# Performance work log

Measured on AMD Instinct MI355X. Metric: run time of the kernel, lower is better.

## Reference

```python
import jax, jax.numpy as jnp
import numpy as np

B, NI, NO = 32, 64, 64


def setup_inputs() -> dict:
    key = jax.random.key(0)
    k1, k2, k3, k4, k5, k6 = jax.random.split(key, 6)
    return {
        "input_re": jax.random.normal(k1, (B, NI, NI), dtype=jnp.float32),
        "input_im": jax.random.normal(k2, (B, NI, NI), dtype=jnp.float32),
        "w_re": jax.random.normal(k3, (NI, NI, NO, NO), dtype=jnp.float32),
        "w_im": jax.random.normal(k4, (NI, NI, NO, NO), dtype=jnp.float32),
        "amp_weights": jax.random.normal(k5, (NI, NI), dtype=jnp.float32),
        "phase_weights": jax.random.normal(k6, (NI, NI), dtype=jnp.float32),
    }


def reference(input_re, input_im, w_re, w_im, amp_weights, phase_weights):
    # complex input field (B, NI, NI) and diffraction kernel (NI, NI, NO, NO)
    e_in = jax.lax.complex(input_re, input_im)
    w_ip = jax.lax.complex(w_re, w_im)
    # passive transmission coefficients: sigmoid(amp) * exp(i*phase)
    ts = (jax.nn.sigmoid(amp_weights)
          * jnp.exp(1j * phase_weights.astype(jnp.complex64))).astype(jnp.complex64)
    # modulated field, then sum over input pixels (i,j) -> complex GEMM
    modulated = e_in * ts[None, :, :]                    # (B, NI, NI)
    out = jnp.einsum('bij,ijkl->bkl', modulated, w_ip)   # (B, NO, NO)
    return out
```

## Files before the change

### kernel.cpp

```cpp
#include <hip/hip_runtime.h>
#include <cstdint>
#include <cstddef>

#define KC 4096
#define NN 4096
#define NB 32
#define HALF (NB * NN)

typedef __attribute__((ext_vector_type(8))) short  bf16x8;
typedef __attribute__((ext_vector_type(16))) float f32x16;

__device__ __forceinline__ unsigned short f2bf(float f) {
    union { float f; unsigned u; } v; v.f = f;
    unsigned r = v.u + 0x7fffu + ((v.u >> 16) & 1u);
    return (unsigned short)(r >> 16);
}

__global__ __launch_bounds__(256) void prep_kernel(
    const float* __restrict__ in_re, const float* __restrict__ in_im,
    const float* __restrict__ amp,   const float* __restrict__ phase,
    uint32_t* __restrict__ wsA)
{
    int tid = blockIdx.x * 256 + threadIdx.x;
    int b = tid >> 12;
    int k = tid & (KC - 1);
    float er = in_re[tid], ei = in_im[tid];
    float a = amp[k], p = phase[k];
    float s = 1.0f / (1.0f + __expf(-a));
    float sn = __sinf(p);
    float cs = __cosf(p);
    float tr = s * cs, ti = s * sn;
    float mr = er * tr - ei * ti;
    float mi = er * ti + ei * tr;
    uint32_t pk = (uint32_t)f2bf(mr) | ((uint32_t)f2bf(mi) << 16);
    wsA[((((k >> 2) << 5) + b) << 2) | (k & 3)] = pk;
}

__global__ __launch_bounds__(256, 4) void gemm_kernel(
    const float* __restrict__ w_re, const float* __restrict__ w_im,
    const uint32_t* __restrict__ wsA, float2* __restrict__ wsP, int steps)
{
    __shared__ float    ldsW[2][2][8][128];
    __shared__ uint32_t ldsA[2][256];

    const int tid  = threadIdx.x;
    const int lane = tid & 63;
    const int wave = tid >> 6;
    const int h    = lane >> 5;
    const int l32  = lane & 31;
    const int n    = blockIdx.x * 128 + wave * 32 + l32;
    const int s    = blockIdx.y;
    const int kbase = s * (steps * 8);

    const int row8 = tid >> 5;
    const int nof  = (tid & 31) << 2;
    const float* gre = w_re + (size_t)(kbase + row8) * NN + blockIdx.x * 128 + nof;
    const float* gim = w_im + (size_t)(kbase + row8) * NN + blockIdx.x * 128 + nof;
    const uint32_t* ga = wsA + (size_t)(kbase >> 2) * 128 + tid;

    f32x16 accR = {};
    f32x16 accI = {};

    auto STAGE = [&](int t, int bb) {
        __builtin_amdgcn_global_load_lds(
            (const __attribute__((address_space(1))) void*)(gre + (size_t)t * 8 * NN),
            (__attribute__((address_space(3))) void*)(&ldsW[bb][0][2 * wave][0]),
            16, 0, 0);
        __builtin_amdgcn_global_load_lds(
            (const __attribute__((address_space(1))) void*)(gim + (size_t)t * 8 * NN),
            (__attribute__((address_space(3))) void*)(&ldsW[bb][1][2 * wave][0]),
            16, 0, 0);
        __builtin_amdgcn_global_load_lds(
            (const __attribute__((address_space(1))) void*)(ga + (size_t)t * 256),
            (__attribute__((address_space(3))) void*)(&ldsA[bb][wave * 64]),
            4, 0, 0);
    };

    auto COMPUTE = [&](int bb) {
        bf16x8 afrag = *(const bf16x8*)&ldsA[bb][h * 128 + l32 * 4];
        const float* Lre = &ldsW[bb][0][h * 4][wave * 32 + l32];
        const float* Lim = &ldsW[bb][1][h * 4][wave * 32 + l32];
        float r0 = Lre[0], r1 = Lre[128], r2 = Lre[256], r3 = Lre[384];
        float i0 = Lim[0], i1 = Lim[128], i2 = Lim[256], i3 = Lim[384];

        bf16x8 bR, bI;
        bR[0] = (short)f2bf(r0);  bR[1] = (short)f2bf(-i0);
        bR[2] = (short)f2bf(r1);  bR[3] = (short)f2bf(-i1);
        bR[4] = (short)f2bf(r2);  bR[5] = (short)f2bf(-i2);
        bR[6] = (short)f2bf(r3);  bR[7] = (short)f2bf(-i3);
        bI[0] = (short)f2bf(i0);  bI[1] = (short)f2bf(r0);
        bI[2] = (short)f2bf(i1);  bI[3] = (short)f2bf(r1);
        bI[4] = (short)f2bf(i2);  bI[5] = (short)f2bf(r2);
        bI[6] = (short)f2bf(i3);  bI[7] = (short)f2bf(r3);

        accR = __builtin_amdgcn_mfma_f32_32x32x16_bf16(afrag, bR, accR, 0, 0, 0);
        accI = __builtin_amdgcn_mfma_f32_32x32x16_bf16(afrag, bI, accI, 0, 0, 0);
    };

    STAGE(0, 0);
    for (int t = 0; t < steps - 1; ++t) {
        STAGE(t + 1, (t + 1) & 1);
        asm volatile("s_waitcnt vmcnt(3)" ::: "memory");
        __builtin_amdgcn_s_barrier();
        COMPUTE(t & 1);
        __builtin_amdgcn_s_barrier();
    }
    asm volatile("s_waitcnt vmcnt(0)" ::: "memory");
    __builtin_amdgcn_s_barrier();
    COMPUTE((steps - 1) & 1);

#pragma unroll
    for (int r = 0; r < 16; ++r) {
        int brow = (r & 3) + 8 * (r >> 2) + 4 * h;
        float2 v; v.x = accR[r]; v.y = accI[r];
        wsP[((size_t)s * NB + brow) * NN + n] = v;
    }
}

__global__ __launch_bounds__(256) void reduce_kernel(
    const float4* __restrict__ wsP, float* __restrict__ out, int S)
{
    int tid = blockIdx.x * 256 + threadIdx.x;
    float re0 = 0.f, im0 = 0.f, re1 = 0.f, im1 = 0.f;
#pragma unroll 8
    for (int s = 0; s < S; ++s) {
        float4 v = wsP[(size_t)s * (NB * NN / 2) + tid];
        re0 += v.x; im0 += v.y; re1 += v.z; im1 += v.w;
    }
    float2* o_re = (float2*)out + tid;
    float2* o_im = (float2*)(out + HALF) + tid;
    *o_re = make_float2(re0, re1);
    *o_im = make_float2(im0, im1);
}

extern "C" void kernel_launch(void* const* d_in, const int* in_sizes, int n_in,
                              void* d_out, int out_size, void* d_ws, size_t ws_size,
                              hipStream_t stream)
{
    const float* in_re  = (const float*)d_in[0];
    const float* in_im  = (const float*)d_in[1];
    const float* w_re   = (const float*)d_in[2];
    const float* w_im   = (const float*)d_in[3];
    const float* amp    = (const float*)d_in[4];
    const float* phase  = (const float*)d_in[5];

    const size_t A_BYTES = (size_t)1024 * 32 * 16;
    uint32_t* wsA = (uint32_t*)d_ws;
    float2*   wsP = (float2*)((char*)d_ws + A_BYTES);

    int S = 32;
    while (S > 1 && A_BYTES + (size_t)S * NB * NN * sizeof(float2) > ws_size) S >>= 1;
    int steps = (KC / S) / 8;

    prep_kernel<<<dim3((NB * KC) / 256), dim3(256), 0, stream>>>(
        in_re, in_im, amp, phase, wsA);

    gemm_kernel<<<dim3(NN / 128, S), dim3(256), 0, stream>>>(
        w_re, w_im, wsA, wsP, steps);

    reduce_kernel<<<dim3((NB * NN / 2) / 256), dim3(256), 0, stream>>>(
        (const float4*)wsP, (float*)d_out, S);
}
```

Before: 170.8 us.

## Deepen GEMM LDS prefetch pipeline to eight buffers and halve split-K

```diff
diff --git a/kernel.cpp b/kernel.cpp
--- a/kernel.cpp
+++ b/kernel.cpp
@@ -6,6 +6,9 @@
 #define NN 4096
 #define NB 32
 #define HALF (NB * NN)
+
+#define NBUF  8
+#define DEPTH 7
 
 typedef __attribute__((ext_vector_type(8))) short  bf16x8;
 typedef __attribute__((ext_vector_type(16))) float f32x16;
@@ -36,12 +39,12 @@
     wsA[((((k >> 2) << 5) + b) << 2) | (k & 3)] = pk;
 }
 
-__global__ __launch_bounds__(256, 4) void gemm_kernel(
+__global__ __launch_bounds__(256, 2) void gemm_kernel(
     const float* __restrict__ w_re, const float* __restrict__ w_im,
     const uint32_t* __restrict__ wsA, float2* __restrict__ wsP, int steps)
 {
-    __shared__ float    ldsW[2][2][8][128];
-    __shared__ uint32_t ldsA[2][256];
+    __shared__ float    ldsW[NBUF][2][8][128];
+    __shared__ uint32_t ldsA[NBUF][256];
 
     const int tid  = threadIdx.x;
     const int lane = tid & 63;
@@ -61,22 +64,25 @@
     f32x16 accR = {};
     f32x16 accI = {};
 
-    auto STAGE = [&](int t, int bb) {
+    auto STAGE = [&](int t) {
+        int tt = t < steps ? t : steps - 1;
+        int bb = t & (NBUF - 1);
         __builtin_amdgcn_global_load_lds(
-            (const __attribute__((address_space(1))) void*)(gre + (size_t)t * 8 * NN),
+            (const __attribute__((address_space(1))) void*)(gre + (size_t)tt * 8 * NN),
             (__attribute__((address_space(3))) void*)(&ldsW[bb][0][2 * wave][0]),
             16, 0, 0);
         __builtin_amdgcn_global_load_lds(
-            (const __attribute__((address_space(1))) void*)(gim + (size_t)t * 8 * NN),
+            (const __attribute__((address_space(1))) void*)(gim + (size_t)tt * 8 * NN),
             (__attribute__((address_space(3))) void*)(&ldsW[bb][1][2 * wave][0]),
             16, 0, 0);
         __builtin_amdgcn_global_load_lds(
-            (const __attribute__((address_space(1))) void*)(ga + (size_t)t * 256),
+            (const __attribute__((address_space(1))) void*)(ga + (size_t)tt * 256),
             (__attribute__((address_space(3))) void*)(&ldsA[bb][wave * 64]),
             4, 0, 0);
     };
 
-    auto COMPUTE = [&](int bb) {
+    auto COMPUTE = [&](int t) {
+        int bb = t & (NBUF - 1);
         bf16x8 afrag = *(const bf16x8*)&ldsA[bb][h * 128 + l32 * 4];
         const float* Lre = &ldsW[bb][0][h * 4][wave * 32 + l32];
         const float* Lim = &ldsW[bb][1][h * 4][wave * 32 + l32];
@@ -97,17 +103,20 @@
         accI = __builtin_amdgcn_mfma_f32_32x32x16_bf16(afrag, bI, accI, 0, 0, 0);
     };
 
-    STAGE(0, 0);
-    for (int t = 0; t < steps - 1; ++t) {
-        STAGE(t + 1, (t + 1) & 1);
-        asm volatile("s_waitcnt vmcnt(3)" ::: "memory");
+#pragma unroll
+    for (int t = 0; t < DEPTH; ++t) STAGE(t);
+
+    for (int t = 0; t < steps - DEPTH; ++t) {
+        STAGE(t + DEPTH);
+        asm volatile("s_waitcnt vmcnt(21)" ::: "memory");
         __builtin_amdgcn_s_barrier();
-        COMPUTE(t & 1);
+        COMPUTE(t);
         __builtin_amdgcn_s_barrier();
     }
+
     asm volatile("s_waitcnt vmcnt(0)" ::: "memory");
     __builtin_amdgcn_s_barrier();
-    COMPUTE((steps - 1) & 1);
+    for (int t = steps - DEPTH; t < steps; ++t) COMPUTE(t);
 
 #pragma unroll
     for (int r = 0; r < 16; ++r) {
@@ -148,7 +157,7 @@
     uint32_t* wsA = (uint32_t*)d_ws;
     float2*   wsP = (float2*)((char*)d_ws + A_BYTES);
 
-    int S = 32;
+    int S = 16;
     while (S > 1 && A_BYTES + (size_t)S * NB * NN * sizeof(float2) > ws_size) S >>= 1;
     int steps = (KC / S) / 8;
 
```

New measurement: 166.5 us. 1.03x faster.

## Widen GEMM tiles to 256 columns and 32-deep K stages with 512 threads

Applied to the files above, without the earlier changes.

```diff
diff --git a/kernel.cpp b/kernel.cpp
--- a/kernel.cpp
+++ b/kernel.cpp
@@ -6,6 +6,7 @@
 #define NN 4096
 #define NB 32
 #define HALF (NB * NN)
+#define KB 32
 
 typedef __attribute__((ext_vector_type(8))) short  bf16x8;
 typedef __attribute__((ext_vector_type(16))) float f32x16;
@@ -36,71 +37,86 @@
     wsA[((((k >> 2) << 5) + b) << 2) | (k & 3)] = pk;
 }
 
-__global__ __launch_bounds__(256, 4) void gemm_kernel(
+__global__ __launch_bounds__(512) void gemm_kernel(
     const float* __restrict__ w_re, const float* __restrict__ w_im,
     const uint32_t* __restrict__ wsA, float2* __restrict__ wsP, int steps)
 {
-    __shared__ float    ldsW[2][2][8][128];
-    __shared__ uint32_t ldsA[2][256];
+    __shared__ float    ldsW[2][2][KB][256];
+    __shared__ uint32_t ldsA[2][KB * 32];
 
     const int tid  = threadIdx.x;
     const int lane = tid & 63;
     const int wave = tid >> 6;
     const int h    = lane >> 5;
     const int l32  = lane & 31;
-    const int n    = blockIdx.x * 128 + wave * 32 + l32;
+    const int n    = blockIdx.x * 256 + wave * 32 + l32;
     const int s    = blockIdx.y;
-    const int kbase = s * (steps * 8);
+    const int kbase = s * (steps * KB);
 
-    const int row8 = tid >> 5;
-    const int nof  = (tid & 31) << 2;
-    const float* gre = w_re + (size_t)(kbase + row8) * NN + blockIdx.x * 128 + nof;
-    const float* gim = w_im + (size_t)(kbase + row8) * NN + blockIdx.x * 128 + nof;
-    const uint32_t* ga = wsA + (size_t)(kbase >> 2) * 128 + tid;
+    const float* gW_re = w_re + (size_t)kbase * NN + blockIdx.x * 256 + (lane << 2);
+    const float* gW_im = w_im + (size_t)kbase * NN + blockIdx.x * 256 + (lane << 2);
+    const uint32_t* gA = wsA + (size_t)(kbase >> 2) * 128 + lane;
 
     f32x16 accR = {};
     f32x16 accI = {};
 
     auto STAGE = [&](int t, int bb) {
-        __builtin_amdgcn_global_load_lds(
-            (const __attribute__((address_space(1))) void*)(gre + (size_t)t * 8 * NN),
-            (__attribute__((address_space(3))) void*)(&ldsW[bb][0][2 * wave][0]),
-            16, 0, 0);
-        __builtin_amdgcn_global_load_lds(
-            (const __attribute__((address_space(1))) void*)(gim + (size_t)t * 8 * NN),
-            (__attribute__((address_space(3))) void*)(&ldsW[bb][1][2 * wave][0]),
-            16, 0, 0);
-        __builtin_amdgcn_global_load_lds(
-            (const __attribute__((address_space(1))) void*)(ga + (size_t)t * 256),
-            (__attribute__((address_space(3))) void*)(&ldsA[bb][wave * 64]),
-            4, 0, 0);
+#pragma unroll
+        for (int j = 0; j < 4; ++j) {
+            int row = j * 8 + wave;
+            __builtin_amdgcn_global_load_lds(
+                (const __attribute__((address_space(1))) void*)(gW_re + (size_t)(t * KB + row) * NN),
+                (__attribute__((address_space(3))) void*)(&ldsW[bb][0][row][0]),
+                16, 0, 0);
+        }
+#pragma unroll
+        for (int j = 0; j < 4; ++j) {
+            int row = j * 8 + wave;
+            __builtin_amdgcn_global_load_lds(
+                (const __attribute__((address_space(1))) void*)(gW_im + (size_t)(t * KB + row) * NN),
+                (__attribute__((address_space(3))) void*)(&ldsW[bb][1][row][0]),
+                16, 0, 0);
+        }
+#pragma unroll
+        for (int j = 0; j < 2; ++j) {
+            int c = wave * 2 + j;
+            __builtin_amdgcn_global_load_lds(
+                (const __attribute__((address_space(1))) void*)(gA + (size_t)t * (KB * 32) + c * 64),
+                (__attribute__((address_space(3))) void*)(&ldsA[bb][c * 64]),
+                4, 0, 0);
+        }
     };
 
     auto COMPUTE = [&](int bb) {
-        bf16x8 afrag = *(const bf16x8*)&ldsA[bb][h * 128 + l32 * 4];
-        const float* Lre = &ldsW[bb][0][h * 4][wave * 32 + l32];
-        const float* Lim = &ldsW[bb][1][h * 4][wave * 32 + l32];
-        float r0 = Lre[0], r1 = Lre[128], r2 = Lre[256], r3 = Lre[384];
-        float i0 = Lim[0], i1 = Lim[128], i2 = Lim[256], i3 = Lim[384];
+#pragma unroll
+        for (int ss = 0; ss < 4; ++ss) {
+            bf16x8 afrag = *(const bf16x8*)&ldsA[bb][ss * 256 + h * 128 + l32 * 4];
+            const float* Lre = &ldsW[bb][0][ss * 8 + h * 4][wave * 32 + l32];
+            const float* Lim = &ldsW[bb][1][ss * 8 + h * 4][wave * 32 + l32];
+            float r0 = Lre[0], r1 = Lre[256], r2 = Lre[512], r3 = Lre[768];
+            float i0 = Lim[0], i1 = Lim[256], i2 = Lim[512], i3 = Lim[768];
 
-        bf16x8 bR, bI;
-        bR[0] = (short)f2bf(r0);  bR[1] = (short)f2bf(-i0);
-        bR[2] = (short)f2bf(r1);  bR[3] = (short)f2bf(-i1);
-        bR[4] = (short)f2bf(r2);  bR[5] = (short)f2bf(-i2);
-        bR[6] = (short)f2bf(r3);  bR[7] = (short)f2bf(-i3);
-        bI[0] = (short)f2bf(i0);  bI[1] = (short)f2bf(r0);
-        bI[2] = (short)f2bf(i1);  bI[3] = (short)f2bf(r1);
-        bI[4] = (short)f2bf(i2);  bI[5] = (short)f2bf(r2);
-        bI[6] = (short)f2bf(i3);  bI[7] = (short)f2bf(r3);
+            unsigned short br0 = f2bf(r0), br1 = f2bf(r1), br2 = f2bf(r2), br3 = f2bf(r3);
+            unsigned short bi0 = f2bf(i0), bi1 = f2bf(i1), bi2 = f2bf(i2), bi3 = f2bf(i3);
+            bf16x8 bR, bI;
+            bR[0] = (short)br0;  bR[1] = (short)(bi0 ^ 0x8000);
+            bR[2] = (short)br1;  bR[3] = (short)(bi1 ^ 0x8000);
+            bR[4] = (short)br2;  bR[5] = (short)(bi2 ^ 0x8000);
+            bR[6] = (short)br3;  bR[7] = (short)(bi3 ^ 0x8000);
+            bI[0] = (short)bi0;  bI[1] = (short)br0;
+            bI[2] = (short)bi1;  bI[3] = (short)br1;
+            bI[4] = (short)bi2;  bI[5] = (short)br2;
+            bI[6] = (short)bi3;  bI[7] = (short)br3;
 
-        accR = __builtin_amdgcn_mfma_f32_32x32x16_bf16(afrag, bR, accR, 0, 0, 0);
-        accI = __builtin_amdgcn_mfma_f32_32x32x16_bf16(afrag, bI, accI, 0, 0, 0);
+            accR = __builtin_amdgcn_mfma_f32_32x32x16_bf16(afrag, bR, accR, 0, 0, 0);
+            accI = __builtin_amdgcn_mfma_f32_32x32x16_bf16(afrag, bI, accI, 0, 0, 0);
+        }
     };
 
     STAGE(0, 0);
     for (int t = 0; t < steps - 1; ++t) {
         STAGE(t + 1, (t + 1) & 1);
-        asm volatile("s_waitcnt vmcnt(3)" ::: "memory");
+        asm volatile("s_waitcnt vmcnt(10)" ::: "memory");
         __builtin_amdgcn_s_barrier();
         COMPUTE(t & 1);
         __builtin_amdgcn_s_barrier();
@@ -148,14 +164,14 @@
     uint32_t* wsA = (uint32_t*)d_ws;
     float2*   wsP = (float2*)((char*)d_ws + A_BYTES);
 
-    int S = 32;
+    int S = 16;
     while (S > 1 && A_BYTES + (size_t)S * NB * NN * sizeof(float2) > ws_size) S >>= 1;
-    int steps = (KC / S) / 8;
+    int steps = (KC / S) / KB;
 
     prep_kernel<<<dim3((NB * KC) / 256), dim3(256), 0, stream>>>(
         in_re, in_im, amp, phase, wsA);
 
-    gemm_kernel<<<dim3(NN / 128, S), dim3(256), 0, stream>>>(
+    gemm_kernel<<<dim3(NN / 256, S), dim3(512), 0, stream>>>(
         w_re, w_im, wsA, wsP, steps);
 
     reduce_kernel<<<dim3((NB * NN / 2) / 256), dim3(256), 0, stream>>>(
```

Result: faster. 164.0 us (-3.9%).
